# Kernel optimization log

Measured on AMD Instinct MI355X. Metric: run time of the kernel, lower is better.

Reference implementation:

```python
import jax, jax.numpy as jnp
import numpy as np

DIM = 256
EXP = 4
EPS_DYT = 1e-5
EPS_ATTN = 1e-5
TEMP = 10000.0


def _linear(x, w, b):
    # torch nn.Linear: y = x @ W^T + b, W is [out, in]
    return jnp.einsum('...i,oi->...o', x, w) + b


def _dwconv3x3(x_nhwc, w, b):
    # depthwise 3x3, padding=1; w: [C,1,3,3]
    xc = x_nhwc.transpose(0, 3, 1, 2)
    y = jax.lax.conv_general_dilated(
        xc, w, window_strides=(1, 1), padding='SAME',
        feature_group_count=w.shape[0],
        dimension_numbers=('NCHW', 'OIHW', 'NCHW'))
    return y.transpose(0, 2, 3, 1) + b


def _dyt(x, gamma, beta):
    mu = x.mean(axis=-1, keepdims=True)
    sd = x.std(axis=-1, keepdims=True, ddof=1) + EPS_DYT  # torch std is unbiased
    return jnp.tanh(gamma * (x - mu) / sd + beta)


def _mona(x, w, b):
    # SE-style: global avg pool -> fc -> sigmoid -> channel gate
    s = jax.nn.sigmoid(_linear(x.mean(axis=(1, 2)), w, b))  # [B,C]
    return x * s[:, None, None, :]


def _pos_emb(H, W, C):
    dq = C // 4
    omega = 1.0 / (TEMP ** (jnp.arange(dq, dtype=jnp.float32) / dq))
    xo = jnp.arange(W, dtype=jnp.float32)[:, None] * omega  # [W,dq]
    yo = jnp.arange(H, dtype=jnp.float32)[:, None] * omega  # [H,dq]
    xe = jnp.concatenate([jnp.sin(xo), jnp.cos(xo)], axis=-1)  # [W,2dq]
    ye = jnp.concatenate([jnp.sin(yo), jnp.cos(yo)], axis=-1)  # [H,2dq]
    pos = jnp.concatenate([
        jnp.broadcast_to(xe[None, :, :], (H, W, 2 * dq)),
        jnp.broadcast_to(ye[:, None, :], (H, W, 2 * dq))], axis=-1)  # [H,W,C]
    return pos


def setup_inputs() -> dict:
    key = jax.random.key(0)
    ks = jax.random.split(key, 16)
    d = DIM
    dh = d * EXP
    w = lambda k, shape: jax.random.normal(k, shape, dtype=jnp.float32) * 0.02
    return {
        'x': jax.random.normal(ks[0], (8, d // 4, 64, 64), dtype=jnp.float32),
        'in_proj_w': w(ks[1], (d, d // 4)),
        'wq_w': w(ks[2], (d, d)), 'wq_b': jnp.zeros((d,), jnp.float32),
        'wk_w': w(ks[3], (d, d)), 'wk_b': jnp.zeros((d,), jnp.float32),
        'wv_w': w(ks[4], (d, d)), 'wv_b': jnp.zeros((d,), jnp.float32),
        'wo_w': w(ks[5], (d, d)), 'wo_b': jnp.zeros((d,), jnp.float32),
        'psi_w': w(ks[6], (d, 1, 3, 3)), 'psi_b': jnp.zeros((d,), jnp.float32),
        'dyt_g': jnp.ones((d,), jnp.float32), 'dyt_b': jnp.zeros((d,), jnp.float32),
        'm1_w': w(ks[7], (d, d)), 'm1_b': jnp.zeros((d,), jnp.float32),
        'm2_w': w(ks[8], (d, d)), 'm2_b': jnp.zeros((d,), jnp.float32),
        'we_w': w(ks[9], (dh, d)), 'we_b': jnp.zeros((dh,), jnp.float32),
        'dw_w': w(ks[10], (dh, 1, 3, 3)), 'dw_b': jnp.zeros((dh,), jnp.float32),
        'wp_w': w(ks[11], (d, dh)), 'wp_b': jnp.zeros((d,), jnp.float32),
        'out_proj_w': w(ks[12], (d // 4, d)),
    }


def _sapa(x, wq_w, wq_b, wk_w, wk_b, wv_w, wv_b, wo_w, wo_b, psi_w, psi_b):
    B, H, W, C = x.shape
    N = H * W
    pos = _pos_emb(H, W, C).reshape(N, C)
    psi = jax.nn.sigmoid(_dwconv3x3(x, psi_w, psi_b)).reshape(B, N, C)
    xf = x.reshape(B, N, C)
    Q = psi * (_linear(xf, wq_w, wq_b) + pos)
    K = psi * (_linear(xf, wk_w, wk_b) + pos)
    V = _linear(xf, wv_w, wv_b)
    phi_Q = jnp.square(jax.nn.relu(Q))
    phi_K = jnp.square(jax.nn.relu(K))
    # attn / (phiQ @ sum_n phiK + eps) @ V  ==  (phiQ @ (phiK^T V)) / (phiQ @ ksum + eps)
    kv = jnp.einsum('bnc,bnd->bcd', phi_K, V)           # [B,C,C]
    num = jnp.einsum('bnc,bcd->bnd', phi_Q, kv)         # [B,N,C]
    den = jnp.einsum('bnc,bc->bn', phi_Q, phi_K.sum(axis=1))[..., None] + EPS_ATTN
    out = _linear(num / den, wo_w, wo_b)
    return out.reshape(B, H, W, C)


def _edffn(x, we_w, we_b, dw_w, dw_b, wp_w, wp_b):
    h = _linear(x, we_w, we_b)                 # [B,H,W,4C]
    h = jax.nn.gelu(_dwconv3x3(h, dw_w, dw_b))
    return x + _linear(h, wp_w, wp_b)


def reference(x, in_proj_w, wq_w, wq_b, wk_w, wk_b, wv_w, wv_b, wo_w, wo_b,
              psi_w, psi_b, dyt_g, dyt_b, m1_w, m1_b, m2_w, m2_b,
              we_w, we_b, dw_w, dw_b, wp_w, wp_b, out_proj_w):
    # in_proj: 1x1 conv (no bias; eval-BN is identity) + SiLU -> NHWC
    h = jax.nn.silu(jnp.einsum('bchw,oc->bhwo', x, in_proj_w))
    a = _sapa(h, wq_w, wq_b, wk_w, wk_b, wv_w, wv_b, wo_w, wo_b, psi_w, psi_b)
    U1 = _mona(_dyt(h + a, dyt_g, dyt_b), m1_w, m1_b)
    U2 = U1 + _edffn(U1, we_w, we_b, dw_w, dw_b, wp_w, wp_b)
    Y = _mona(_dyt(U2, dyt_g, dyt_b), m2_w, m2_b)
    return jax.nn.silu(jnp.einsum('bhwc,oc->bohw', Y, out_proj_w))
```

## Files before the change

kernel.cpp:

```cpp
#include <hip/hip_runtime.h>
#include <hip/hip_bf16.h>
#include <cmath>

using bf16 = __hip_bfloat16;
using bf16x8 = __attribute__((ext_vector_type(8))) short;
using bf16x4 = __attribute__((ext_vector_type(4))) short;
using f32x4v = __attribute__((ext_vector_type(4))) float;

static constexpr int BB  = 8;
static constexpr int HW  = 64;
static constexpr int NN  = HW * HW;
static constexpr int CC  = 256;
static constexpr int CIN = 64;
static constexpr int DH  = 1024;
static constexpr int MM  = BB * NN;

__device__ __forceinline__ bf16 f2b(float v) { return __float2bfloat16(v); }
__device__ __forceinline__ float b2f(bf16 v) { return __bfloat162float(v); }
__device__ __forceinline__ float tf(float v) { return v; }
__device__ __forceinline__ float tf(bf16 v)  { return b2f(v); }
__device__ __forceinline__ float frcp(float x) { return __builtin_amdgcn_rcpf(x); }
__device__ __forceinline__ float sigmf(float x) { return frcp(1.f + __expf(-x)); }
__device__ __forceinline__ float siluf(float x) { return x * sigmf(x); }
__device__ __forceinline__ float geluf(float x) {
  float z = x * fmaf(x * x, 0.07135481627f, 1.5957691216f);
  return x * sigmf(z);
}
__device__ __forceinline__ float tanhfast(float x) {
  return 1.f - 2.f * frcp(1.f + __expf(2.f * x));
}

__device__ __forceinline__ void stage16(const bf16* g, bf16* l) {
  __builtin_amdgcn_global_load_lds(
      (const __attribute__((address_space(1))) void*)g,
      (__attribute__((address_space(3))) void*)l, 16, 0, 0);
}

__global__ __launch_bounds__(256) void pos_kern(float* __restrict__ pos) {
  int n = blockIdx.x, o = threadIdx.x;
  int yy = n >> 6, xx = n & 63;
  int i = o & 63, q = o >> 6;
  float omega = __expf((float)i * -0.14391156831212787f);
  float coord = (q < 2) ? (float)xx : (float)yy;
  float ang = coord * omega;
  pos[(size_t)n * CC + o] = (q & 1) ? __cosf(ang) : __sinf(ang);
}

__global__ __launch_bounds__(256) void cvt_weights(
    const float* __restrict__ wq, const float* __restrict__ wk,
    const float* __restrict__ wv, const float* __restrict__ wo,
    const float* __restrict__ we, const float* __restrict__ wp,
    const float* __restrict__ qb, const float* __restrict__ kb,
    const float* __restrict__ vb,
    bf16* __restrict__ wqkvb, bf16* __restrict__ wob,
    bf16* __restrict__ web, bf16* __restrict__ wpb,
    float* __restrict__ bqkv, float* __restrict__ ksum) {
  int i = blockIdx.x * 256 + threadIdx.x;
  switch (blockIdx.y) {
    case 0: if (i < 65536) wqkvb[i] = f2b(wq[i]);
            if (i < 2048) ksum[i] = 0.f;
            break;
    case 1: if (i < 65536) wqkvb[65536 + i] = f2b(wk[i]);
            if (i < 768) bqkv[i] = (i < 256) ? qb[i] : (i < 512) ? kb[i - 256] : vb[i - 512];
            break;
    case 2: if (i < 65536) wqkvb[131072 + i] = f2b(wv[i]); break;
    case 3: if (i < 65536) wob[i] = f2b(wo[i]); break;
    case 4: web[i] = f2b(we[i]); break;
    case 5: wpb[i] = f2b(wp[i]); break;
  }
}

__global__ __launch_bounds__(256) void inproj_tile(const float* __restrict__ X,
                                                   const float* __restrict__ W,
                                                   bf16* __restrict__ Hb) {
  __shared__ float Xs[16][68];
  __shared__ float Ws[16][68];
  int m0 = blockIdx.x * 64, o0 = blockIdx.y * 64, b = blockIdx.z;
  int tid = threadIdx.x, tx = tid & 15, ty = tid >> 4;
  float acc[4][4] = {};
  for (int k0 = 0; k0 < CIN; k0 += 16) {
    {
      int mm = tid & 63, kk0 = tid >> 6;
#pragma unroll
      for (int i = 0; i < 4; ++i) {
        int kk = kk0 * 4 + i;
        Xs[kk][mm] = X[((size_t)(b * CIN + k0 + kk)) * NN + m0 + mm];
      }
    }
    {
      int kk = tid & 15, oo0 = tid >> 4;
#pragma unroll
      for (int i = 0; i < 4; ++i) {
        int oo = oo0 + i * 16;
        Ws[kk][oo] = W[(size_t)(o0 + oo) * CIN + k0 + kk];
      }
    }
    __syncthreads();
#pragma unroll
    for (int kk = 0; kk < 16; ++kk) {
      float xv[4], wv[4];
#pragma unroll
      for (int a = 0; a < 4; ++a) xv[a] = Xs[kk][ty * 4 + a];
#pragma unroll
      for (int c = 0; c < 4; ++c) wv[c] = Ws[kk][tx * 4 + c];
#pragma unroll
      for (int a = 0; a < 4; ++a)
#pragma unroll
        for (int c = 0; c < 4; ++c) acc[a][c] += xv[a] * wv[c];
    }
    __syncthreads();
  }
#pragma unroll
  for (int a = 0; a < 4; ++a) {
    int m = m0 + ty * 4 + a;
#pragma unroll
    for (int c = 0; c < 4; ++c) {
      int o = o0 + tx * 4 + c;
      float v = siluf(acc[a][c]);
      Hb[((size_t)b * NN + m) * CC + o] = f2b(v);
    }
  }
}

__global__ __launch_bounds__(256) void outproj_tile(const float* __restrict__ A,
                                                    const float2* __restrict__ stats,
                                                    const float* __restrict__ gate,
                                                    const float* __restrict__ gdyt,
                                                    const float* __restrict__ bdyt,
                                                    const float* __restrict__ W,
                                                    float* __restrict__ Y) {
  __shared__ float Xs[16][68];
  __shared__ float Ws[16][68];
  int n0 = blockIdx.x * 64, b = blockIdx.z;
  size_t mbase = (size_t)b * NN;
  const float* gb = gate + b * CC;
  int tid = threadIdx.x, tx = tid & 15, ty = tid >> 4;
  float acc[4][4] = {};
  for (int k0 = 0; k0 < CC; k0 += 16) {
    int kk = tid & 15, rr0 = tid >> 4;
    float gk = gb[k0 + kk];
    float gd = gdyt[k0 + kk];
    float bd = bdyt[k0 + kk];
#pragma unroll
    for (int i = 0; i < 4; ++i) {
      int rr = rr0 + i * 16;
      size_t m = mbase + n0 + rr;
      float2 st = stats[m];
      float xv = A[m * CC + k0 + kk];
      Xs[kk][rr] = tanhfast(fmaf(gd * (xv - st.x), st.y, bd)) * gk;
      Ws[kk][rr] = (rr < CIN) ? W[(size_t)rr * CC + k0 + kk] : 0.f;
    }
    __syncthreads();
#pragma unroll
    for (int kk2 = 0; kk2 < 16; ++kk2) {
      float xv[4], wv[4];
#pragma unroll
      for (int a = 0; a < 4; ++a) xv[a] = Xs[kk2][ty * 4 + a];
#pragma unroll
      for (int c = 0; c < 4; ++c) wv[c] = Ws[kk2][tx * 4 + c];
#pragma unroll
      for (int a = 0; a < 4; ++a)
#pragma unroll
        for (int c = 0; c < 4; ++c) acc[a][c] += xv[a] * wv[c];
    }
    __syncthreads();
  }
#pragma unroll
  for (int a = 0; a < 4; ++a) {
    int n = n0 + ty * 4 + a;
#pragma unroll
    for (int c = 0; c < 4; ++c) {
      int o = tx * 4 + c;
      if (o < CIN)
        Y[(size_t)(b * CIN + o) * NN + n] = siluf(acc[a][c]);
    }
  }
}

enum { EPI_PLAIN = 0, EPI_BIAS = 1, EPI_NUM = 3, EPI_RESID = 4, EPI_ADD1 = 5 };

__device__ __forceinline__ void storeO(float* p, float v) { *p = v; }
__device__ __forceinline__ void storeO(bf16* p, float v) { *p = f2b(v); }

template <int EPI, bool WPB, bool KVS, bool XSWZ, typename YT, typename A2T>
__global__ __launch_bounds__(256) void gemm_bf16(const bf16* __restrict__ X,
                                                 const bf16* __restrict__ W,
                                                 const float* __restrict__ bias,
                                                 YT* __restrict__ Y, int Kd, int Od,
                                                 const float* __restrict__ aux1,
                                                 const A2T* __restrict__ aux2) {
  __shared__ __align__(16) bf16 As[128 * 32];
  __shared__ __align__(16) bf16 Bs[128 * 32];
  int m0, o0;
  if (XSWZ) {
    int gy = gridDim.y;
    int nwg = gridDim.x * gy;
    int lin = blockIdx.y * gridDim.x + blockIdx.x;
    int q = nwg >> 3;
    int lin2 = (lin & 7) * q + (lin >> 3);
    m0 = (lin2 / gy) * 128;
    o0 = (lin2 % gy) * 128;
  } else {
    m0 = blockIdx.x * 128;
    o0 = blockIdx.y * 128;
  }
  int kbeg = 0, kend = Kd;
  if (KVS) {
    int b = blockIdx.z >> 4, ks = blockIdx.z & 15;
    size_t off = (size_t)b * CC * Kd;
    X += off; W += off;
    Y += (size_t)blockIdx.z * CC * CC;
    kbeg = ks * (Kd / 16); kend = kbeg + Kd / 16;
  }
  const bf16* Wp = WPB ? (W + (size_t)(m0 >> 12) * Kd * Od) : W;
  int t = threadIdx.x;
  int l = t & 63, w = t >> 6;
  int wm = (w >> 1) * 64, wn = (w & 1) * 64;
  int lr = l & 15, lq = l >> 4;
  int srow = t >> 2, skc = (t & 3) * 8;
  f32x4v acc[4][4] = {};
  for (int k0 = kbeg; k0 < kend; k0 += 32) {
    stage16(X + (size_t)(m0 + srow) * Kd + k0 + skc, As + t * 8);
    stage16(X + (size_t)(m0 + 64 + srow) * Kd + k0 + skc, As + 2048 + t * 8);
    stage16(Wp + (size_t)(o0 + srow) * Kd + k0 + skc, Bs + t * 8);
    stage16(Wp + (size_t)(o0 + 64 + srow) * Kd + k0 + skc, Bs + 2048 + t * 8);
    __syncthreads();
    bf16x8 af[4], bfr[4];
#pragma unroll
    for (int mt = 0; mt < 4; ++mt)
      af[mt] = *(const bf16x8*)(As + (wm + mt * 16 + lr) * 32 + lq * 8);
#pragma unroll
    for (int nt = 0; nt < 4; ++nt)
      bfr[nt] = *(const bf16x8*)(Bs + (wn + nt * 16 + lr) * 32 + lq * 8);
#pragma unroll
    for (int mt = 0; mt < 4; ++mt)
#pragma unroll
      for (int nt = 0; nt < 4; ++nt)
        acc[mt][nt] = __builtin_amdgcn_mfma_f32_16x16x32_bf16(af[mt], bfr[nt], acc[mt][nt], 0, 0, 0);
    __syncthreads();
  }
#pragma unroll
  for (int nt = 0; nt < 4; ++nt) {
    int o = o0 + wn + nt * 16 + lr;
    float bv = (EPI == EPI_PLAIN || EPI == EPI_NUM) ? 0.f : bias[o];
#pragma unroll
    for (int mt = 0; mt < 4; ++mt) {
      int mb = m0 + wm + mt * 16 + lq * 4;
#pragma unroll
      for (int r = 0; r < 4; ++r) {
        int m = mb + r;
        float v = acc[mt][nt][r] + bv;
        if constexpr (EPI == EPI_PLAIN || EPI == EPI_BIAS) {
          storeO(Y + (size_t)m * Od + o, v);
        } else if constexpr (EPI == EPI_NUM) {
          storeO(Y + (size_t)m * Od + o, v * aux1[m]);
        } else if constexpr (EPI == EPI_ADD1) {
          storeO(Y + (size_t)m * Od + o, v + tf(aux2[(size_t)m * Od + o]));
        } else {
          storeO(Y + (size_t)m * Od + o, v + 2.f * tf(aux2[(size_t)m * Od + o]));
        }
      }
    }
  }
}

__global__ __launch_bounds__(256) void qkmath_kern(const bf16* __restrict__ QKV,
                                                   const float* __restrict__ pose,
                                                   const bf16* __restrict__ psi,
                                                   bf16* __restrict__ PQ,
                                                   bf16* __restrict__ KT,
                                                   bf16* __restrict__ VTo,
                                                   float* __restrict__ ksum) {
  __shared__ bf16 Ts[64][258];
  int sec = blockIdx.y;
  int m0 = blockIdx.x * 64;
  int b = m0 >> 12, n0 = m0 & (NN - 1);
  int t = threadIdx.x;
  int cg = (t & 31) * 8;
  int rg = t >> 5;
  if (sec == 0) {
#pragma unroll
    for (int p = 0; p < 8; ++p) {
      int r = p * 8 + rg;
      size_t m = (size_t)m0 + r;
      int n = (int)(m & (NN - 1));
      union { bf16x8 v; bf16 e[8]; } qv, pv, ov;
      qv.v = *(const bf16x8*)(QKV + m * 768 + cg);
      pv.v = *(const bf16x8*)(psi + m * CC + cg);
      const float* pr = pose + (size_t)n * CC + cg;
      f32x4v p0 = *(const f32x4v*)pr;
      f32x4v p1 = *(const f32x4v*)(pr + 4);
#pragma unroll
      for (int j = 0; j < 8; ++j) {
        float pj = (j < 4) ? p0[j] : p1[j - 4];
        float v = (b2f(qv.e[j]) + pj) * b2f(pv.e[j]);
        v = fmaxf(v, 0.f);
        ov.e[j] = f2b(v * v);
      }
      *(bf16x8*)(PQ + m * CC + cg) = ov.v;
    }
    return;
  }
  const bool KM = (sec == 1);
#pragma unroll
  for (int p = 0; p < 8; ++p) {
    int r = p * 8 + rg;
    size_t m = (size_t)m0 + r;
    union { bf16x8 v; bf16 e[8]; } qv, ov;
    qv.v = *(const bf16x8*)(QKV + m * 768 + sec * 256 + cg);
    if (KM) {
      int n = (int)(m & (NN - 1));
      union { bf16x8 v; bf16 e[8]; } pv;
      pv.v = *(const bf16x8*)(psi + m * CC + cg);
      const float* pr = pose + (size_t)n * CC + cg;
      f32x4v p0 = *(const f32x4v*)pr;
      f32x4v p1 = *(const f32x4v*)(pr + 4);
#pragma unroll
      for (int j = 0; j < 8; ++j) {
        float pj = (j < 4) ? p0[j] : p1[j - 4];
        float v = (b2f(qv.e[j]) + pj) * b2f(pv.e[j]);
        v = fmaxf(v, 0.f);
        ov.e[j] = f2b(v * v);
      }
    } else {
      ov.v = qv.v;
    }
    *(bf16x8*)(&Ts[r][cg]) = ov.v;
  }
  __syncthreads();
  int wv = t >> 6, lane = t & 63;
  bf16* base = KM ? KT : VTo;
  int nloc = (lane & 7) * 8;
  int gsub = lane >> 3;
#pragma unroll
  for (int k = 0; k < 8; ++k) {
    int c = wv * 64 + k * 8 + gsub;
    union { bf16x8 v; bf16 e[8]; } pk;
#pragma unroll
    for (int i = 0; i < 8; ++i) pk.e[i] = Ts[nloc + i][c];
    *(bf16x8*)(base + ((size_t)(b * CC + c)) * NN + n0 + nloc) = pk.v;
    if (KM) {
      float s = 0.f;
#pragma unroll
      for (int i = 0; i < 8; ++i) s += b2f(pk.e[i]);
      s += __shfl_xor(s, 1);
      s += __shfl_xor(s, 2);
      s += __shfl_xor(s, 4);
      if ((lane & 7) == 0) atomicAdd(&ksum[b * CC + c], s);
    }
  }
}

__global__ __launch_bounds__(256) void kvred_kern(const bf16* __restrict__ part,
                                                  bf16* __restrict__ kvTb) {
  int d = blockIdx.x, b = blockIdx.y, c = threadIdx.x;
  float s = 0.f;
#pragma unroll
  for (int ks = 0; ks < 16; ++ks)
    s += b2f(part[((size_t)(b * 16 + ks) * CC + d) * CC + c]);
  kvTb[((size_t)b * CC + d) * CC + c] = f2b(s);
}

__global__ __launch_bounds__(256) void den_kern(const bf16* __restrict__ PQ,
                                                const float* __restrict__ ksum,
                                                float* __restrict__ rden) {
  int b = blockIdx.y;
  int n = blockIdx.x * 4 + (threadIdx.x >> 6);
  int lane = threadIdx.x & 63;
  size_t m = (size_t)b * NN + n;
  union { bf16x4 v; bf16 e[4]; } u;
  u.v = *(const bf16x4*)(PQ + m * CC + lane * 4);
  const float* ks = ksum + b * CC + lane * 4;
  float s = 0.f;
#pragma unroll
  for (int j = 0; j < 4; ++j) s += b2f(u.e[j]) * ks[j];
#pragma unroll
  for (int off = 32; off >= 1; off >>= 1) s += __shfl_down(s, off);
  if (lane == 0) rden[m] = 1.f / (s + 1e-5f);
}

__global__ __launch_bounds__(256) void dytstat_kern(const float* __restrict__ X,
                                                    const float* __restrict__ g,
                                                    const float* __restrict__ bt,
                                                    float2* __restrict__ stats,
                                                    float* __restrict__ poolq) {
  int wv = threadIdx.x >> 6;
  int m = blockIdx.x * 4 + wv;
  int lane = threadIdx.x & 63;
  size_t base = (size_t)m * CC + lane * 4;
  f32x4v x = *(const f32x4v*)(X + base);
  float s = (x[0] + x[1]) + (x[2] + x[3]);
  float q = fmaf(x[0], x[0], fmaf(x[1], x[1], fmaf(x[2], x[2], x[3] * x[3])));
#pragma unroll
  for (int off = 32; off >= 1; off >>= 1) {
    s += __shfl_xor(s, off);
    q += __shfl_xor(q, off);
  }
  float mu = s * (1.f / 256.f);
  float var = (q - 256.f * mu * mu) * (1.f / 255.f);
  float sd = sqrtf(fmaxf(var, 0.f)) + 1e-5f;
  float rs = frcp(sd);
  if (lane == 0) stats[m] = make_float2(mu, rs);
  f32x4v gv = *(const f32x4v*)(g + lane * 4);
  f32x4v bv = *(const f32x4v*)(bt + lane * 4);
  f32x4v o;
#pragma unroll
  for (int j = 0; j < 4; ++j)
    o[j] = tanhfast(fmaf(gv[j] * (x[j] - mu), rs, bv[j]));
  __shared__ float ps[4][260];
#pragma unroll
  for (int j = 0; j < 4; ++j) ps[wv][lane * 4 + j] = o[j];
  __syncthreads();
  if (wv == 0) {
    f32x4v pv;
#pragma unroll
    for (int j = 0; j < 4; ++j) {
      int c = lane * 4 + j;
      pv[j] = (ps[0][c] + ps[1][c]) + (ps[2][c] + ps[3][c]);
    }
    *(f32x4v*)(poolq + (size_t)blockIdx.x * 256 + lane * 4) = pv;
  }
}

__global__ __launch_bounds__(256) void poolred_kern(const float* __restrict__ poolq,
                                                    float* __restrict__ pool16) {
  int s = blockIdx.x, b = blockIdx.y, c = threadIdx.x;
  float acc = 0.f;
#pragma unroll 8
  for (int k = 0; k < 64; ++k)
    acc += poolq[((size_t)(b * 1024 + s * 64 + k)) * 256 + c];
  pool16[(size_t)(b * 16 + s) * 256 + c] = acc;
}

__global__ __launch_bounds__(256) void gate_kern(const float* __restrict__ pool16,
                                                 const float* __restrict__ w,
                                                 const float* __restrict__ bias,
                                                 float* __restrict__ gate) {
  int b = blockIdx.x, o = threadIdx.x;
  __shared__ float p[CC];
  float s = 0.f;
#pragma unroll
  for (int k = 0; k < 16; ++k) s += pool16[(size_t)(b * 16 + k) * 256 + o];
  p[o] = s * (1.f / 4096.f);
  __syncthreads();
  float acc = bias[o];
  for (int c = 0; c < CC; ++c) acc += p[c] * w[o * CC + c];
  gate[b * CC + o] = sigmf(acc);
}

__global__ __launch_bounds__(256) void scale_from_A(const float* __restrict__ X,
                                                    const float2* __restrict__ stats,
                                                    const float* __restrict__ gate,
                                                    const float* __restrict__ g,
                                                    const float* __restrict__ bt,
                                                    bf16* __restrict__ Ob) {
  int wv = threadIdx.x >> 6;
  int m = blockIdx.x * 4 + wv;
  int lane = threadIdx.x & 63;
  int b = m >> 12;
  size_t base = (size_t)m * CC + lane * 4;
  f32x4v x = *(const f32x4v*)(X + base);
  float2 st = stats[m];
  f32x4v gv = *(const f32x4v*)(g + lane * 4);
  f32x4v bv = *(const f32x4v*)(bt + lane * 4);
  f32x4v gg = *(const f32x4v*)(gate + b * CC + lane * 4);
  union { bf16x4 v; bf16 e[4]; } ob;
#pragma unroll
  for (int j = 0; j < 4; ++j) {
    float tv = tanhfast(fmaf(gv[j] * (x[j] - st.x), st.y, bv[j]));
    ob.e[j] = f2b(tv * gg[j]);
  }
  *(bf16x4*)(Ob + base) = ob.v;
}

template <int STRIDE>
__device__ __forceinline__ void dw_loadrow_b16(float (&row)[3][4], const bf16* __restrict__ Xb,
                                               int yy, int x, int dl, int dr) {
  if (yy < 0 || yy >= HW) {
#pragma unroll
    for (int cx = 0; cx < 3; ++cx)
#pragma unroll
      for (int j = 0; j < 4; ++j) row[cx][j] = 0.f;
    return;
  }
  const bf16* base = Xb + ((size_t)yy * HW + x) * (size_t)STRIDE;
  union U { bf16x4 v; bf16 e[4]; } um, ul, ur;
  um.v = *(const bf16x4*)base;
  ul.v = *(const bf16x4*)(base + dl);
  ur.v = *(const bf16x4*)(base + dr);
#pragma unroll
  for (int j = 0; j < 4; ++j) {
    row[0][j] = b2f(ul.e[j]);
    row[1][j] = b2f(um.e[j]);
    row[2][j] = b2f(ur.e[j]);
  }
}

__global__ __launch_bounds__(256) void dwconv_psi_v2(const bf16* __restrict__ X,
                                                     const float* __restrict__ w,
                                                     const float* __restrict__ bias,
                                                     bf16* __restrict__ Y) {
  int i = blockIdx.x;
  int lin = (i & 7) * 64 + (i >> 3);
  int xg = lin & 15, yc = (lin >> 4) & 3, b = lin >> 6;
  int c0 = (threadIdx.x & 63) * 4;
  int x  = xg * 4 + (threadIdx.x >> 6);
  int y0 = yc * 16;
  const bf16* Xb = X + (size_t)b * NN * CC + c0;
  bf16* Yb      = Y + (size_t)b * NN * CC + c0;
  float wt[9][4], bs[4];
#pragma unroll
  for (int j = 0; j < 4; ++j) {
    bs[j] = bias[c0 + j];
#pragma unroll
    for (int t9 = 0; t9 < 9; ++t9) wt[t9][j] = w[(c0 + j) * 9 + t9];
  }
  const bool xl = (x > 0), xr = (x < HW - 1);
  if (!xl) {
#pragma unroll
    for (int j = 0; j < 4; ++j) wt[0][j] = wt[3][j] = wt[6][j] = 0.f;
  }
  if (!xr) {
#pragma unroll
    for (int j = 0; j < 4; ++j) wt[2][j] = wt[5][j] = wt[8][j] = 0.f;
  }
  const int dl = xl ? -CC : 0, dr = xr ? CC : 0;
  float win[5][3][4];
  dw_loadrow_b16<CC>(win[0], Xb, y0 - 1, x, dl, dr);
  dw_loadrow_b16<CC>(win[1], Xb, y0,     x, dl, dr);
  dw_loadrow_b16<CC>(win[2], Xb, y0 + 1, x, dl, dr);
  dw_loadrow_b16<CC>(win[3], Xb, y0 + 2, x, dl, dr);
#pragma unroll
  for (int ii = 0; ii < 16; ++ii) {
    dw_loadrow_b16<CC>(win[(ii + 4) % 5], Xb, y0 + ii + 3, x, dl, dr);
    const int rt = ii % 5, rm = (ii + 1) % 5, rb = (ii + 2) % 5;
    union { bf16x4 v; bf16 e[4]; } o;
#pragma unroll
    for (int j = 0; j < 4; ++j) {
      float a = bs[j];
#pragma unroll
      for (int cx = 0; cx < 3; ++cx) {
        a = fmaf(win[rt][cx][j], wt[cx][j], a);
        a = fmaf(win[rm][cx][j], wt[3 + cx][j], a);
        a = fmaf(win[rb][cx][j], wt[6 + cx][j], a);
      }
      o.e[j] = f2b(sigmf(a));
    }
    *(bf16x4*)(Yb + ((size_t)(y0 + ii) * HW + x) * (size_t)CC) = o.v;
  }
}

__global__ __launch_bounds__(256) void dwconv1024_v2(const bf16* __restrict__ X,
                                                     const float* __restrict__ w,
                                                     const float* __restrict__ bias,
                                                     bf16* __restrict__ Y) {
  int i = blockIdx.x;
  int lin = (i & 7) * 256 + (i >> 3);
  int x = lin & 63, yc = (lin >> 6) & 3, b = lin >> 8;
  int c0 = threadIdx.x * 4;
  int y0 = yc * 16;
  const bf16* Xb = X + (size_t)b * NN * DH + c0;
  bf16* Yb       = Y + (size_t)b * NN * DH + c0;
  float wt[9][4], bs[4];
#pragma unroll
  for (int j = 0; j < 4; ++j) {
    bs[j] = bias[c0 + j];
#pragma unroll
    for (int t9 = 0; t9 < 9; ++t9) wt[t9][j] = w[(c0 + j) * 9 + t9];
  }
  const bool xl = (x > 0), xr = (x < HW - 1);
  if (!xl) {
#pragma unroll
    for (int j = 0; j < 4; ++j) wt[0][j] = wt[3][j] = wt[6][j] = 0.f;
  }
  if (!xr) {
#pragma unroll
    for (int j = 0; j < 4; ++j) wt[2][j] = wt[5][j] = wt[8][j] = 0.f;
  }
  const int dl = xl ? -DH : 0, dr = xr ? DH : 0;
  float win[5][3][4];
  dw_loadrow_b16<DH>(win[0], Xb, y0 - 1, x, dl, dr);
  dw_loadrow_b16<DH>(win[1], Xb, y0,     x, dl, dr);
  dw_loadrow_b16<DH>(win[2], Xb, y0 + 1, x, dl, dr);
  dw_loadrow_b16<DH>(win[3], Xb, y0 + 2, x, dl, dr);
#pragma unroll
  for (int ii = 0; ii < 16; ++ii) {
    dw_loadrow_b16<DH>(win[(ii + 4) % 5], Xb, y0 + ii + 3, x, dl, dr);
    const int rt = ii % 5, rm = (ii + 1) % 5, rb = (ii + 2) % 5;
    union { bf16x4 v; bf16 e[4]; } o;
#pragma unroll
    for (int j = 0; j < 4; ++j) {
      float a = bs[j];
#pragma unroll
      for (int cx = 0; cx < 3; ++cx) {
        a = fmaf(win[rt][cx][j], wt[cx][j], a);
        a = fmaf(win[rm][cx][j], wt[3 + cx][j], a);
        a = fmaf(win[rb][cx][j], wt[6 + cx][j], a);
      }
      o.e[j] = f2b(geluf(a));
    }
    *(bf16x4*)(Yb + ((size_t)(y0 + ii) * HW + x) * (size_t)DH) = o.v;
  }
}

extern "C" void kernel_launch(void* const* d_in, const int* in_sizes, int n_in,
                              void* d_out, int out_size, void* d_ws, size_t ws_size,
                              hipStream_t stream) {
  (void)in_sizes; (void)n_in; (void)out_size; (void)ws_size;
  const float* x       = (const float*)d_in[0];
  const float* in_proj = (const float*)d_in[1];
  const float* wq_w = (const float*)d_in[2];   const float* wq_b = (const float*)d_in[3];
  const float* wk_w = (const float*)d_in[4];   const float* wk_b = (const float*)d_in[5];
  const float* wv_w = (const float*)d_in[6];   const float* wv_b = (const float*)d_in[7];
  const float* wo_w = (const float*)d_in[8];   const float* wo_b = (const float*)d_in[9];
  const float* psi_w = (const float*)d_in[10]; const float* psi_b = (const float*)d_in[11];
  const float* dyt_g = (const float*)d_in[12]; const float* dyt_b = (const float*)d_in[13];
  const float* m1_w = (const float*)d_in[14];  const float* m1_b = (const float*)d_in[15];
  const float* m2_w = (const float*)d_in[16];  const float* m2_b = (const float*)d_in[17];
  const float* we_w = (const float*)d_in[18];  const float* we_b = (const float*)d_in[19];
  const float* dw_w = (const float*)d_in[20];  const float* dw_b = (const float*)d_in[21];
  const float* wp_w = (const float*)d_in[22];  const float* wp_b = (const float*)d_in[23];
  const float* wout = (const float*)d_in[24];
  float* out = (float*)d_out;

  char* ws = (char*)d_ws;
  const size_t MB = 1u << 20;
  float* A     = (float*)(ws + 32 * MB);
  bf16*  psiB  = (bf16*)(ws + 64 * MB);
  bf16*  numb  = (bf16*)(ws + 80 * MB);
  bf16*  phiQ  = (bf16*)(ws + 96 * MB);
  bf16*  Hb    = (bf16*)(ws + 112 * MB);
  bf16*  phiKT = (bf16*)(ws + 128 * MB);
  bf16*  VT    = (bf16*)(ws + 144 * MB);
  bf16*  QKVr  = (bf16*)(ws + 160 * MB);
  bf16*  kvpartB = (bf16*)(ws + 160 * MB);
  bf16*  e1    = (bf16*)(ws + 64 * MB);
  bf16*  e2    = (bf16*)(ws + 128 * MB);
  bf16*  U1b   = (bf16*)(ws + 192 * MB);
  bf16* wqkvb = (bf16*)(ws + 208 * MB);
  bf16* wob   = wqkvb + 196608;
  bf16* web   = wob + 65536;
  bf16* wpb   = web + 262144;
  float* bqkv = (float*)(wpb + 262144);
  float* pose = (float*)(ws + 210 * MB);
  char*  small = ws + 214 * MB;
  float* ksum  = (float*)(small);
  float* rden  = (float*)(small + 64 * 1024);
  float* pool16 = (float*)(small + 192 * 1024);
  float* gate1 = (float*)(small + 704 * 1024);
  float* gate2 = (float*)(small + 720 * 1024);
  bf16*  kvTb  = (bf16*)(small + 768 * 1024);
  float* poolq = (float*)(ws + 216 * MB);
  float2* stats1 = (float2*)(ws + 224 * MB);
  float2* stats2 = (float2*)(ws + 225 * MB);

  dim3 blk(256);

  pos_kern<<<dim3(NN), blk, 0, stream>>>(pose);
  cvt_weights<<<dim3(1024, 6), blk, 0, stream>>>(wq_w, wk_w, wv_w, wo_w, we_w, wp_w,
                                                 wq_b, wk_b, wv_b,
                                                 wqkvb, wob, web, wpb, bqkv, ksum);
  inproj_tile<<<dim3(64, 4, BB), blk, 0, stream>>>(x, in_proj, Hb);

  dwconv_psi_v2<<<dim3(512), blk, 0, stream>>>(Hb, psi_w, psi_b, psiB);
  gemm_bf16<EPI_BIAS, false, false, true, bf16, float>
      <<<dim3(256, 6), blk, 0, stream>>>(Hb, wqkvb, bqkv, QKVr, CC, 768, nullptr, nullptr);
  qkmath_kern<<<dim3(MM / 64, 3), blk, 0, stream>>>(QKVr, pose, psiB, phiQ, phiKT, VT, ksum);
  gemm_bf16<EPI_PLAIN, false, true, false, bf16, float>
      <<<dim3(2, 2, 128), blk, 0, stream>>>(VT, phiKT, nullptr, kvpartB, NN, CC, nullptr, nullptr);
  kvred_kern<<<dim3(CC, BB), blk, 0, stream>>>(kvpartB, kvTb);
  den_kern<<<dim3(1024, BB), blk, 0, stream>>>(phiQ, ksum, rden);
  gemm_bf16<EPI_NUM, true, false, true, bf16, float>
      <<<dim3(256, 2), blk, 0, stream>>>(phiQ, kvTb, nullptr, numb, CC, CC, rden, nullptr);
  gemm_bf16<EPI_ADD1, false, false, true, float, bf16>
      <<<dim3(256, 2), blk, 0, stream>>>(numb, wob, wo_b, A, CC, CC, nullptr, Hb);

  dytstat_kern<<<dim3(MM / 4), blk, 0, stream>>>(A, dyt_g, dyt_b, stats1, poolq);
  poolred_kern<<<dim3(16, BB), blk, 0, stream>>>(poolq, pool16);
  gate_kern<<<dim3(BB), blk, 0, stream>>>(pool16, m1_w, m1_b, gate1);
  scale_from_A<<<dim3(MM / 4), blk, 0, stream>>>(A, stats1, gate1, dyt_g, dyt_b, U1b);

  gemm_bf16<EPI_BIAS, false, false, true, bf16, float>
      <<<dim3(256, 8), blk, 0, stream>>>(U1b, web, we_b, e1, CC, DH, nullptr, nullptr);
  dwconv1024_v2<<<dim3(2048), blk, 0, stream>>>(e1, dw_w, dw_b, e2);
  gemm_bf16<EPI_RESID, false, false, true, float, bf16>
      <<<dim3(256, 2), blk, 0, stream>>>(e2, wpb, wp_b, A, DH, CC, nullptr, U1b);

  dytstat_kern<<<dim3(MM / 4), blk, 0, stream>>>(A, dyt_g, dyt_b, stats2, poolq);
  poolred_kern<<<dim3(16, BB), blk, 0, stream>>>(poolq, pool16);
  gate_kern<<<dim3(BB), blk, 0, stream>>>(pool16, m2_w, m2_b, gate2);

  outproj_tile<<<dim3(64, 1, BB), blk, 0, stream>>>(A, stats2, gate2, dyt_g, dyt_b, wout, out);
}
```

Before: 422.4 us.

## Fold output projection into per-batch KV matrix to skip one full GEMM

Reassociates (phiQ·kv)·Wo^T into phiQ·(kv·Wo^T). A small batched GEMM first builds a per-batch combined 256x256 matrix from Wo and the transposed kv, and a single large GEMM over all tokens then applies it with the denominator scale, bias and residual in its epilogue. This removes one full-size token GEMM plus the write and re-read of the intermediate numerator buffer. The cost is an extra small batched GEMM, a transposed store in the kv reduction, and rounding the combined matrix to bf16, which changes numerics slightly.

```diff
diff --git a/kernel.cpp b/kernel.cpp
--- a/kernel.cpp
+++ b/kernel.cpp
@@ -177,12 +177,12 @@
   }
 }
 
-enum { EPI_PLAIN = 0, EPI_BIAS = 1, EPI_NUM = 3, EPI_RESID = 4, EPI_ADD1 = 5 };
+enum { EPI_PLAIN = 0, EPI_BIAS = 1, EPI_NUM = 3, EPI_RESID = 4, EPI_ADD1 = 5, EPI_NUMADD = 6 };
 
 __device__ __forceinline__ void storeO(float* p, float v) { *p = v; }
 __device__ __forceinline__ void storeO(bf16* p, float v) { *p = f2b(v); }
 
-template <int EPI, bool WPB, bool KVS, bool XSWZ, typename YT, typename A2T>
+template <int EPI, bool WPB, bool KVS, bool XSWZ, bool BATW, typename YT, typename A2T>
 __global__ __launch_bounds__(256) void gemm_bf16(const bf16* __restrict__ X,
                                                  const bf16* __restrict__ W,
                                                  const float* __restrict__ bias,
@@ -212,6 +212,10 @@
     Y += (size_t)blockIdx.z * CC * CC;
     kbeg = ks * (Kd / 16); kend = kbeg + Kd / 16;
   }
+  if (BATW) {
+    W += (size_t)blockIdx.z * Kd * Od;
+    Y += (size_t)blockIdx.z * Kd * Od;
+  }
   const bf16* Wp = WPB ? (W + (size_t)(m0 >> 12) * Kd * Od) : W;
   int t = threadIdx.x;
   int l = t & 63, w = t >> 6;
@@ -242,7 +246,7 @@
 #pragma unroll
   for (int nt = 0; nt < 4; ++nt) {
     int o = o0 + wn + nt * 16 + lr;
-    float bv = (EPI == EPI_PLAIN || EPI == EPI_NUM) ? 0.f : bias[o];
+    float bv = (EPI == EPI_PLAIN || EPI == EPI_NUM || EPI == EPI_NUMADD) ? 0.f : bias[o];
 #pragma unroll
     for (int mt = 0; mt < 4; ++mt) {
       int mb = m0 + wm + mt * 16 + lq * 4;
@@ -254,6 +258,8 @@
           storeO(Y + (size_t)m * Od + o, v);
         } else if constexpr (EPI == EPI_NUM) {
           storeO(Y + (size_t)m * Od + o, v * aux1[m]);
+        } else if constexpr (EPI == EPI_NUMADD) {
+          storeO(Y + (size_t)m * Od + o, v * aux1[m] + bias[o] + tf(aux2[(size_t)m * Od + o]));
         } else if constexpr (EPI == EPI_ADD1) {
           storeO(Y + (size_t)m * Od + o, v + tf(aux2[(size_t)m * Od + o]));
         } else {
@@ -352,13 +358,13 @@
 }
 
 __global__ __launch_bounds__(256) void kvred_kern(const bf16* __restrict__ part,
-                                                  bf16* __restrict__ kvTb) {
+                                                  bf16* __restrict__ kvTc) {
   int d = blockIdx.x, b = blockIdx.y, c = threadIdx.x;
   float s = 0.f;
 #pragma unroll
   for (int ks = 0; ks < 16; ++ks)
     s += b2f(part[((size_t)(b * 16 + ks) * CC + d) * CC + c]);
-  kvTb[((size_t)b * CC + d) * CC + c] = f2b(s);
+  kvTc[((size_t)b * CC + c) * CC + d] = f2b(s);
 }
 
 __global__ __launch_bounds__(256) void den_kern(const bf16* __restrict__ PQ,
@@ -627,7 +633,6 @@
   const size_t MB = 1u << 20;
   float* A     = (float*)(ws + 32 * MB);
   bf16*  psiB  = (bf16*)(ws + 64 * MB);
-  bf16*  numb  = (bf16*)(ws + 80 * MB);
   bf16*  phiQ  = (bf16*)(ws + 96 * MB);
   bf16*  Hb    = (bf16*)(ws + 112 * MB);
   bf16*  phiKT = (bf16*)(ws + 128 * MB);
@@ -649,10 +654,11 @@
   float* pool16 = (float*)(small + 192 * 1024);
   float* gate1 = (float*)(small + 704 * 1024);
   float* gate2 = (float*)(small + 720 * 1024);
-  bf16*  kvTb  = (bf16*)(small + 768 * 1024);
+  bf16*  kvTc  = (bf16*)(small + 768 * 1024);
   float* poolq = (float*)(ws + 216 * MB);
   float2* stats1 = (float2*)(ws + 224 * MB);
   float2* stats2 = (float2*)(ws + 225 * MB);
+  bf16*  Mb    = (bf16*)(ws + 226 * MB);
 
   dim3 blk(256);
 
@@ -663,27 +669,27 @@
   inproj_tile<<<dim3(64, 4, BB), blk, 0, stream>>>(x, in_proj, Hb);
 
   dwconv_psi_v2<<<dim3(512), blk, 0, stream>>>(Hb, psi_w, psi_b, psiB);
-  gemm_bf16<EPI_BIAS, false, false, true, bf16, float>
+  gemm_bf16<EPI_BIAS, false, false, true, false, bf16, float>
       <<<dim3(256, 6), blk, 0, stream>>>(Hb, wqkvb, bqkv, QKVr, CC, 768, nullptr, nullptr);
   qkmath_kern<<<dim3(MM / 64, 3), blk, 0, stream>>>(QKVr, pose, psiB, phiQ, phiKT, VT, ksum);
-  gemm_bf16<EPI_PLAIN, false, true, false, bf16, float>
+  gemm_bf16<EPI_PLAIN, false, true, false, false, bf16, float>
       <<<dim3(2, 2, 128), blk, 0, stream>>>(VT, phiKT, nullptr, kvpartB, NN, CC, nullptr, nullptr);
-  kvred_kern<<<dim3(CC, BB), blk, 0, stream>>>(kvpartB, kvTb);
+  kvred_kern<<<dim3(CC, BB), blk, 0, stream>>>(kvpartB, kvTc);
   den_kern<<<dim3(1024, BB), blk, 0, stream>>>(phiQ, ksum, rden);
-  gemm_bf16<EPI_NUM, true, false, true, bf16, float>
-      <<<dim3(256, 2), blk, 0, stream>>>(phiQ, kvTb, nullptr, numb, CC, CC, rden, nullptr);
-  gemm_bf16<EPI_ADD1, false, false, true, float, bf16>
-      <<<dim3(256, 2), blk, 0, stream>>>(numb, wob, wo_b, A, CC, CC, nullptr, Hb);
+  gemm_bf16<EPI_PLAIN, false, false, false, true, bf16, float>
+      <<<dim3(2, 2, BB), blk, 0, stream>>>(wob, kvTc, nullptr, Mb, CC, CC, nullptr, nullptr);
+  gemm_bf16<EPI_NUMADD, true, false, true, false, float, bf16>
+      <<<dim3(256, 2), blk, 0, stream>>>(phiQ, Mb, wo_b, A, CC, CC, rden, Hb);
 
   dytstat_kern<<<dim3(MM / 4), blk, 0, stream>>>(A, dyt_g, dyt_b, stats1, poolq);
   poolred_kern<<<dim3(16, BB), blk, 0, stream>>>(poolq, pool16);
   gate_kern<<<dim3(BB), blk, 0, stream>>>(pool16, m1_w, m1_b, gate1);
   scale_from_A<<<dim3(MM / 4), blk, 0, stream>>>(A, stats1, gate1, dyt_g, dyt_b, U1b);
 
-  gemm_bf16<EPI_BIAS, false, false, true, bf16, float>
+  gemm_bf16<EPI_BIAS, false, false, true, false, bf16, float>
       <<<dim3(256, 8), blk, 0, stream>>>(U1b, web, we_b, e1, CC, DH, nullptr, nullptr);
   dwconv1024_v2<<<dim3(2048), blk, 0, stream>>>(e1, dw_w, dw_b, e2);
-  gemm_bf16<EPI_RESID, false, false, true, float, bf16>
+  gemm_bf16<EPI_RESID, false, false, true, false, float, bf16>
       <<<dim3(256, 2), blk, 0, stream>>>(e2, wpb, wp_b, A, DH, CC, nullptr, U1b);
 
   dytstat_kern<<<dim3(MM / 4), blk, 0, stream>>>(A, dyt_g, dyt_b, stats2, poolq);
```

After: 435.1 us. 3.0% more time.
